# Kernel tuning notes

Measured on AMD Instinct MI355X. Metric: run time of the kernel, lower is better.

The kernel has to match this reference:

```python
import jax, jax.numpy as jnp
import numpy as np

D_MODEL = 1024
NUM_HEADS = 16
HEAD_DIM = D_MODEL // NUM_HEADS
SCALE = HEAD_DIM ** -0.5


def setup_inputs() -> dict:
    key = jax.random.key(0)
    k1, k2, k3, k4 = jax.random.split(key, 4)
    B, N = 4, 2048
    x = jax.random.normal(k1, (B, N, D_MODEL), dtype=jnp.float32)
    # nn.Linear weights: stored as (out, in); apply as x @ W.T
    w_qkv = jax.random.normal(k2, (3 * D_MODEL, D_MODEL), dtype=jnp.float32) * (D_MODEL ** -0.5)
    w_proj = jax.random.normal(k3, (D_MODEL, D_MODEL), dtype=jnp.float32) * (D_MODEL ** -0.5)
    b_proj = jax.random.normal(k4, (D_MODEL,), dtype=jnp.float32) * 0.02
    return {"x": x, "w_qkv": w_qkv, "w_proj": w_proj, "b_proj": b_proj}


def reference(x, w_qkv, w_proj, b_proj):
    B, N, C = x.shape
    qkv = jnp.einsum('bnc,dc->bnd', x, w_qkv)            # [B, N, 3C]
    qkv = qkv.reshape(B, N, 3, NUM_HEADS, HEAD_DIM)
    qkv = jnp.transpose(qkv, (2, 0, 3, 1, 4))             # [3, B, H, N, hd]
    q, k, v = qkv[0], qkv[1], qkv[2]
    q = q * SCALE
    attn = jnp.einsum('bhnd,bhmd->bhnm', q, k)            # [B, H, N, N]
    attn = jax.nn.softmax(attn, axis=-1)
    out = jnp.einsum('bhnm,bhmd->bhnd', attn, v)          # [B, H, N, hd]
    out = jnp.transpose(out, (0, 2, 1, 3)).reshape(B, N, C)
    return jnp.einsum('bnc,dc->bnd', out, w_proj) + b_proj
```

## Files before the change

kernel.cpp:

```cpp
#include <hip/hip_runtime.h>
#include <hip/hip_bf16.h>
#include <stdint.h>

#define D_MODEL 1024
#define NHEADS  16
#define HDIM    64
#define BATCH   4
#define SEQ     2048
#define NTOK    (BATCH*SEQ)
#define QSCALE  0.125f
#define LOG2E   1.4426950408889634f
#define FIXED_M 16.0f

typedef __attribute__((ext_vector_type(8)))  short bf16x8;
typedef __attribute__((ext_vector_type(4)))  float f32x4;
typedef __attribute__((ext_vector_type(16))) float f32x16;

static __device__ __forceinline__ unsigned short f2bf(float f) {
    union { float f; unsigned u; } v; v.f = f;
    unsigned r = v.u + 0x7FFFu + ((v.u >> 16) & 1u);
    return (unsigned short)(r >> 16);
}

static __device__ __forceinline__ unsigned cvtpk_bf16(float lo, float hi) {
    unsigned r;
    asm("v_cvt_pk_bf16_f32 %0, %1, %2" : "=v"(r) : "v"(lo), "v"(hi));
    return r;
}

static __device__ __forceinline__ float fast_exp2(float x) {
    float r;
    asm("v_exp_f32 %0, %1" : "=v"(r) : "v"(x));
    return r;
}

#define GLDS16(g, l) __builtin_amdgcn_global_load_lds( \
    (const __attribute__((address_space(1))) void*)(g), \
    (__attribute__((address_space(3))) void*)(l), 16, 0, 0)

__global__ void cvt_kernel(const float* __restrict__ in,
                           unsigned short* __restrict__ out, int n4) {
    int i = blockIdx.x * blockDim.x + threadIdx.x;
    int stride = gridDim.x * blockDim.x;
    for (; i < n4; i += stride) {
        f32x4 v = *(const f32x4*)(in + (size_t)i * 4);
        ushort4 o;
        o.x = f2bf(v.x); o.y = f2bf(v.y); o.z = f2bf(v.z); o.w = f2bf(v.w);
        *(ushort4*)(out + (size_t)i * 4) = o;
    }
}

#define BM 128
#define BN 128
#define BK 64

template<int MODE>
__global__ __launch_bounds__(256, 2) void gemm_nt(
    const unsigned short* __restrict__ A,
    const unsigned short* __restrict__ B,
    int M, int N, int K,
    unsigned short* __restrict__ Qb, unsigned short* __restrict__ Kb,
    unsigned short* __restrict__ Vb,
    float* __restrict__ Out, const float* __restrict__ bias)
{
    __shared__ __attribute__((aligned(16))) unsigned short As[BM * BK];
    __shared__ __attribute__((aligned(16))) unsigned short Bs[BN * BK];

    const int bn = blockIdx.x, bm = blockIdx.y;
    const int tid = threadIdx.x;
    const int wid = tid >> 6, lane = tid & 63;
    const int wm = wid >> 1, wn = wid & 1;
    const int lr = lane & 15, lg = lane >> 4;

    const unsigned short* Ablk = A + (size_t)bm * BM * K;
    const unsigned short* Bblk = B + (size_t)bn * BN * K;

    f32x4 acc[4][4] = {};

    for (int k0 = 0; k0 < K; k0 += BK) {
#pragma unroll
        for (int r = 0; r < 4; ++r) {
            const int chunk = wid * 4 + r;
            const int row = chunk * 8 + (lane >> 3);
            const int colk = k0 + (lane & 7) * 8;
            GLDS16(Ablk + (size_t)row * K + colk, As + chunk * 512);
            GLDS16(Bblk + (size_t)row * K + colk, Bs + chunk * 512);
        }
        __syncthreads();
#pragma unroll
        for (int kk = 0; kk < BK / 32; ++kk) {
            bf16x8 af[4], bfr[4];
#pragma unroll
            for (int m = 0; m < 4; ++m)
                af[m] = *(const bf16x8*)(As + (wm * 64 + m * 16 + lr) * BK + kk * 32 + lg * 8);
#pragma unroll
            for (int n = 0; n < 4; ++n)
                bfr[n] = *(const bf16x8*)(Bs + (wn * 64 + n * 16 + lr) * BK + kk * 32 + lg * 8);
#pragma unroll
            for (int m = 0; m < 4; ++m)
#pragma unroll
                for (int n = 0; n < 4; ++n)
                    acc[m][n] = __builtin_amdgcn_mfma_f32_16x16x32_bf16(
                        af[m], bfr[n], acc[m][n], 0, 0, 0);
        }
        __syncthreads();
    }

    const int row0 = bm * BM + wm * 64;
    const int col0 = bn * BN + wn * 64;
#pragma unroll
    for (int m = 0; m < 4; ++m) {
#pragma unroll
        for (int n = 0; n < 4; ++n) {
            const int row = row0 + m * 16 + lg * 4;
            const int col = col0 + n * 16 + lr;
            if (MODE == 0) {
                const int which = col >> 10;
                const int h = (col >> 6) & 15;
                const int e = col & 63;
                const int b = row >> 11;
                const int s = row & (SEQ - 1);
                if (which == 2) {
                    const int sp = (s & ~12) | ((s & 4) << 1) | ((s & 8) >> 1);
                    ushort4 w;
                    w.x = f2bf(acc[m][n][0]); w.y = f2bf(acc[m][n][1]);
                    w.z = f2bf(acc[m][n][2]); w.w = f2bf(acc[m][n][3]);
                    *(ushort4*)(Vb + ((size_t)((b * NHEADS + h) * HDIM + e)) * SEQ + sp) = w;
                } else {
                    unsigned short* dst = (which == 0) ? Qb : Kb;
                    const float sc = (which == 0) ? (QSCALE * LOG2E) : 1.0f;
                    const size_t base = ((size_t)(b * NHEADS + h) * SEQ + s) * HDIM + e;
#pragma unroll
                    for (int r = 0; r < 4; ++r)
                        dst[base + (size_t)r * HDIM] = f2bf(acc[m][n][r] * sc);
                }
            } else {
                const float bv = bias[col];
#pragma unroll
                for (int r = 0; r < 4; ++r)
                    Out[(size_t)(row + r) * N + col] = acc[m][n][r] + bv;
            }
        }
    }
}


__global__ __launch_bounds__(256, 2) void flash_fwd9(
    const unsigned short* __restrict__ Q,
    const unsigned short* __restrict__ Kg,
    const unsigned short* __restrict__ Vt,
    unsigned short* __restrict__ Ob)
{
    __shared__ __attribute__((aligned(16))) unsigned short Kl[3][64 * 64];
    __shared__ __attribute__((aligned(16))) unsigned short Vl[3][64 * 64];

    const int bid = blockIdx.x;
    const int xcd = bid & 7;
    const int ord = bid >> 3;
    const int bh  = xcd * 8 + (ord >> 3);
    const int qt  = ord & 7;

    const int wid  = threadIdx.x >> 6;
    const int lane = threadIdx.x & 63;
    const int col = lane & 31;
    const int hi  = lane >> 5;

    const size_t bhoff = (size_t)bh * SEQ * HDIM;
    const unsigned short* Qp = Q + bhoff;
    const unsigned short* Kp = Kg + bhoff;
    const unsigned short* Vp = Vt + bhoff;

    const int q0 = qt * 256 + wid * 64;

    const int r8  = lane >> 3;
    const int swe = ((lane & 7) ^ r8) << 3;
    auto stage_kv = [&](unsigned short* Kld, unsigned short* Vld, int k0) {
#pragma unroll
        for (int i = 0; i < 2; ++i) {
            const int chunk = wid * 2 + i;
            const int row = chunk * 8 + r8;
            GLDS16(Kp + (size_t)(k0 + row) * HDIM + swe, Kld + chunk * 512);
            GLDS16(Vp + (size_t)row * SEQ + k0 + swe, Vld + chunk * 512);
        }
    };

    bf16x8 qf[2][4];
#pragma unroll
    for (int mt = 0; mt < 2; ++mt)
#pragma unroll
        for (int c = 0; c < 4; ++c)
            qf[mt][c] = *(const bf16x8*)(Qp + (size_t)(q0 + mt * 32 + col) * HDIM + c * 16 + hi * 8);

    f32x16 o[2][2] = {};
    float lacc[2] = { 0.f, 0.f };

    const int swr = (col & 7) << 4;
    auto compute_tile = [&](const unsigned short* Kld, const unsigned short* Vld) {
#pragma unroll
        for (int sub = 0; sub < 2; ++sub) {
            const int key = sub * 32 + col;
            bf16x8 kf[4];
#pragma unroll
            for (int c = 0; c < 4; ++c)
                kf[c] = *(const bf16x8*)((const char*)Kld + key * 128 +
                                         ((c * 32 + hi * 16) ^ swr));
            f32x16 s[2] = {};
#pragma unroll
            for (int c = 0; c < 4; ++c) {
                s[0] = __builtin_amdgcn_mfma_f32_32x32x16_bf16(kf[c], qf[0][c], s[0], 0, 0, 0);
                s[1] = __builtin_amdgcn_mfma_f32_32x32x16_bf16(kf[c], qf[1][c], s[1], 0, 0, 0);
            }
            bf16x8 vA[2][2];
#pragma unroll
            for (int ks = 0; ks < 2; ++ks)
#pragma unroll
                for (int nt = 0; nt < 2; ++nt)
                    vA[ks][nt] = *(const bf16x8*)((const char*)Vld + (nt * 32 + col) * 128 +
                                                  ((sub * 64 + ks * 32 + hi * 16) ^ swr));
#pragma unroll
            for (int mt = 0; mt < 2; ++mt) {
                float p[16]; float rs = 0.f;
#pragma unroll
                for (int i = 0; i < 16; ++i) {
                    p[i] = fast_exp2(s[mt][i] - FIXED_M);
                    rs += p[i];
                }
                lacc[mt] += rs;
                union { unsigned w[4]; bf16x8 v; } f0, f1;
#pragma unroll
                for (int d = 0; d < 4; ++d) {
                    f0.w[d] = cvtpk_bf16(p[2 * d],     p[2 * d + 1]);
                    f1.w[d] = cvtpk_bf16(p[8 + 2 * d], p[9 + 2 * d]);
                }
#pragma unroll
                for (int nt = 0; nt < 2; ++nt) {
                    o[mt][nt] = __builtin_amdgcn_mfma_f32_32x32x16_bf16(vA[0][nt], f0.v, o[mt][nt], 0, 0, 0);
                    o[mt][nt] = __builtin_amdgcn_mfma_f32_32x32x16_bf16(vA[1][nt], f1.v, o[mt][nt], 0, 0, 0);
                }
            }
        }
    };

    unsigned short *kb0 = Kl[0], *kb1 = Kl[1], *kb2 = Kl[2];
    unsigned short *vb0 = Vl[0], *vb1 = Vl[1], *vb2 = Vl[2];
    stage_kv(kb0, vb0, 0);
    stage_kv(kb1, vb1, 64);

    for (int t = 0; t < SEQ / 64; ++t) {
        asm volatile("s_waitcnt vmcnt(4)" ::: "memory");
        __builtin_amdgcn_s_barrier();
        stage_kv(kb2, vb2, ((t + 2) & 31) * 64);
        compute_tile(kb0, vb0);
        asm volatile("s_waitcnt lgkmcnt(0)" ::: "memory");
        unsigned short* tk = kb0; kb0 = kb1; kb1 = kb2; kb2 = tk;
        unsigned short* tv = vb0; vb0 = vb1; vb1 = vb2; vb2 = tv;
    }

    const int b = bh >> 4, h = bh & 15;
#pragma unroll
    for (int mt = 0; mt < 2; ++mt) {
        const float ls = lacc[mt] + __shfl_xor(lacc[mt], 32);
        const float inv = 1.0f / ls;
        const size_t tok = (size_t)b * SEQ + q0 + mt * 32 + col;
#pragma unroll
        for (int nt = 0; nt < 2; ++nt)
#pragma unroll
            for (int rq = 0; rq < 4; ++rq) {
                ushort4 w;
                w.x = f2bf(o[mt][nt][rq * 4 + 0] * inv);
                w.y = f2bf(o[mt][nt][rq * 4 + 1] * inv);
                w.z = f2bf(o[mt][nt][rq * 4 + 2] * inv);
                w.w = f2bf(o[mt][nt][rq * 4 + 3] * inv);
                *(ushort4*)(Ob + tok * D_MODEL + h * HDIM + nt * 32 + rq * 8 + hi * 4) = w;
            }
    }
}

extern "C" void kernel_launch(void* const* d_in, const int* in_sizes, int n_in,
                              void* d_out, int out_size, void* d_ws, size_t ws_size,
                              hipStream_t stream)
{
    const float* x      = (const float*)d_in[0];
    const float* w_qkv  = (const float*)d_in[1];
    const float* w_proj = (const float*)d_in[2];
    const float* b_proj = (const float*)d_in[3];
    float* out = (float*)d_out;

    char* ws = (char*)d_ws;
    size_t off = 0;
    auto alloc = [&](size_t elems) -> unsigned short* {
        unsigned short* p = (unsigned short*)(ws + off);
        off += ((elems * 2 + 255) & ~(size_t)255);
        return p;
    };
    unsigned short* xb  = alloc((size_t)NTOK * D_MODEL);
    unsigned short* wqb = alloc((size_t)3 * D_MODEL * D_MODEL);
    unsigned short* wpb = alloc((size_t)D_MODEL * D_MODEL);
    unsigned short* Qb  = alloc((size_t)NTOK * D_MODEL);
    unsigned short* Kb  = alloc((size_t)NTOK * D_MODEL);
    unsigned short* Vb  = alloc((size_t)NTOK * D_MODEL);
    unsigned short* Ab  = alloc((size_t)NTOK * D_MODEL);

    cvt_kernel<<<2048, 256, 0, stream>>>(x, xb, NTOK * D_MODEL / 4);
    cvt_kernel<<<1024, 256, 0, stream>>>(w_qkv, wqb, 3 * D_MODEL * D_MODEL / 4);
    cvt_kernel<<<256, 256, 0, stream>>>(w_proj, wpb, D_MODEL * D_MODEL / 4);

    gemm_nt<0><<<dim3(3 * D_MODEL / BN, NTOK / BM), 256, 0, stream>>>(
        xb, wqb, NTOK, 3 * D_MODEL, D_MODEL, Qb, Kb, Vb, nullptr, nullptr);

    flash_fwd9<<<dim3(512), 256, 0, stream>>>(Qb, Kb, Vb, Ab);

    gemm_nt<1><<<dim3(D_MODEL / BN, NTOK / BM), 256, 0, stream>>>(
        Ab, wpb, NTOK, D_MODEL, D_MODEL, nullptr, nullptr, nullptr, out, b_proj);
}
```

Baseline: 196.4 us.

## Double-buffer GEMM LDS tiles with XOR swizzle and merge conversion kernels

The GEMM now keeps two LDS buffers per operand and issues the global-to-LDS loads for the next K tile before computing the current one, using explicit vmcnt waits and raw barriers. This overlaps the memory loads with the MFMA work. The global source columns are XOR-swizzled per row, and the LDS reads apply the matching XOR, to spread accesses across LDS banks. The three fp32-to-bf16 conversion launches are merged into one kernel to cut launch overhead. The cost is twice the LDS per block, which may reduce occupancy, plus hand-written waitcnt logic that must match the number of loads issued.

```diff
diff --git a/kernel.cpp b/kernel.cpp
--- a/kernel.cpp
+++ b/kernel.cpp
@@ -38,15 +38,28 @@
     (const __attribute__((address_space(1))) void*)(g), \
     (__attribute__((address_space(3))) void*)(l), 16, 0, 0)
 
-__global__ void cvt_kernel(const float* __restrict__ in,
-                           unsigned short* __restrict__ out, int n4) {
+#define N4_X   (NTOK * D_MODEL / 4)
+#define N4_WQ  (3 * D_MODEL * D_MODEL / 4)
+#define N4_WP  (D_MODEL * D_MODEL / 4)
+
+__global__ void cvt_all(const float* __restrict__ x,
+                        const float* __restrict__ wq,
+                        const float* __restrict__ wp,
+                        unsigned short* __restrict__ xb,
+                        unsigned short* __restrict__ wqb,
+                        unsigned short* __restrict__ wpb) {
+    const int total = N4_X + N4_WQ + N4_WP;
     int i = blockIdx.x * blockDim.x + threadIdx.x;
-    int stride = gridDim.x * blockDim.x;
-    for (; i < n4; i += stride) {
-        f32x4 v = *(const f32x4*)(in + (size_t)i * 4);
+    const int stride = gridDim.x * blockDim.x;
+    for (; i < total; i += stride) {
+        const float* src; unsigned short* dst; int j;
+        if (i < N4_X)             { src = x;  dst = xb;  j = i; }
+        else if (i < N4_X + N4_WQ){ src = wq; dst = wqb; j = i - N4_X; }
+        else                      { src = wp; dst = wpb; j = i - N4_X - N4_WQ; }
+        f32x4 v = *(const f32x4*)(src + (size_t)j * 4);
         ushort4 o;
         o.x = f2bf(v.x); o.y = f2bf(v.y); o.z = f2bf(v.z); o.w = f2bf(v.w);
-        *(ushort4*)(out + (size_t)i * 4) = o;
+        *(ushort4*)(dst + (size_t)j * 4) = o;
     }
 }
 
@@ -63,8 +76,8 @@
     unsigned short* __restrict__ Vb,
     float* __restrict__ Out, const float* __restrict__ bias)
 {
-    __shared__ __attribute__((aligned(16))) unsigned short As[BM * BK];
-    __shared__ __attribute__((aligned(16))) unsigned short Bs[BN * BK];
+    __shared__ __attribute__((aligned(16))) unsigned short As[2][BM * BK];
+    __shared__ __attribute__((aligned(16))) unsigned short Bs[2][BN * BK];
 
     const int bn = blockIdx.x, bm = blockIdx.y;
     const int tid = threadIdx.x;
@@ -75,27 +88,45 @@
     const unsigned short* Ablk = A + (size_t)bm * BM * K;
     const unsigned short* Bblk = B + (size_t)bn * BN * K;
 
-    f32x4 acc[4][4] = {};
-
-    for (int k0 = 0; k0 < K; k0 += BK) {
+    const int swe = ((lane & 7) ^ (lane >> 3)) << 3;
+    const int r8  = lane >> 3;
+
+    auto stage = [&](int buf, int k0) {
 #pragma unroll
         for (int r = 0; r < 4; ++r) {
             const int chunk = wid * 4 + r;
-            const int row = chunk * 8 + (lane >> 3);
-            const int colk = k0 + (lane & 7) * 8;
-            GLDS16(Ablk + (size_t)row * K + colk, As + chunk * 512);
-            GLDS16(Bblk + (size_t)row * K + colk, Bs + chunk * 512);
-        }
-        __syncthreads();
+            const int row = chunk * 8 + r8;
+            GLDS16(Ablk + (size_t)row * K + k0 + swe, As[buf] + chunk * 512);
+            GLDS16(Bblk + (size_t)row * K + k0 + swe, Bs[buf] + chunk * 512);
+        }
+    };
+
+    f32x4 acc[4][4] = {};
+
+    const int NT = K / BK;
+    stage(0, 0);
+    for (int t = 0; t < NT; ++t) {
+        if (t + 1 < NT) {
+            stage((t + 1) & 1, (t + 1) * BK);
+            asm volatile("s_waitcnt vmcnt(8)" ::: "memory");
+        } else {
+            asm volatile("s_waitcnt vmcnt(0)" ::: "memory");
+        }
+        __builtin_amdgcn_s_barrier();
+
+        const int cb = t & 1;
+        const int swr = (lr & 7) << 4;
 #pragma unroll
         for (int kk = 0; kk < BK / 32; ++kk) {
             bf16x8 af[4], bfr[4];
 #pragma unroll
             for (int m = 0; m < 4; ++m)
-                af[m] = *(const bf16x8*)(As + (wm * 64 + m * 16 + lr) * BK + kk * 32 + lg * 8);
+                af[m] = *(const bf16x8*)((const char*)As[cb] +
+                        (wm * 64 + m * 16 + lr) * 128 + ((kk * 64 + lg * 16) ^ swr));
 #pragma unroll
             for (int n = 0; n < 4; ++n)
-                bfr[n] = *(const bf16x8*)(Bs + (wn * 64 + n * 16 + lr) * BK + kk * 32 + lg * 8);
+                bfr[n] = *(const bf16x8*)((const char*)Bs[cb] +
+                        (wn * 64 + n * 16 + lr) * 128 + ((kk * 64 + lg * 16) ^ swr));
 #pragma unroll
             for (int m = 0; m < 4; ++m)
 #pragma unroll
@@ -103,7 +134,8 @@
                     acc[m][n] = __builtin_amdgcn_mfma_f32_16x16x32_bf16(
                         af[m], bfr[n], acc[m][n], 0, 0, 0);
         }
-        __syncthreads();
+        asm volatile("s_waitcnt lgkmcnt(0)" ::: "memory");
+        __builtin_amdgcn_s_barrier();
     }
 
     const int row0 = bm * BM + wm * 64;
@@ -144,7 +176,6 @@
     }
 }
 
-
 __global__ __launch_bounds__(256, 2) void flash_fwd9(
     const unsigned short* __restrict__ Q,
     const unsigned short* __restrict__ Kg,
@@ -301,9 +332,7 @@
     unsigned short* Vb  = alloc((size_t)NTOK * D_MODEL);
     unsigned short* Ab  = alloc((size_t)NTOK * D_MODEL);
 
-    cvt_kernel<<<2048, 256, 0, stream>>>(x, xb, NTOK * D_MODEL / 4);
-    cvt_kernel<<<1024, 256, 0, stream>>>(w_qkv, wqb, 3 * D_MODEL * D_MODEL / 4);
-    cvt_kernel<<<256, 256, 0, stream>>>(w_proj, wpb, D_MODEL * D_MODEL / 4);
+    cvt_all<<<2048, 256, 0, stream>>>(x, w_qkv, w_proj, xb, wqb, wpb);
 
     gemm_nt<0><<<dim3(3 * D_MODEL / BN, NTOK / BM), 256, 0, stream>>>(
         xb, wqb, NTOK, 3 * D_MODEL, D_MODEL, Qb, Kb, Vb, nullptr, nullptr);
```

Measured after the change: 186.6 us (median of 2 runs). 5.0% less time.
